# Kernel optimization log

Measured on AMD Instinct MI355X. Metric: run time of the kernel, lower is better.

The kernel has to match this reference:

```python
import jax, jax.numpy as jnp
import numpy as np

NUM_GRAPHS = 1024


def setup_inputs() -> dict:
    key = jax.random.key(0)
    k1, k2, k3, k4 = jax.random.split(key, 4)
    N, D = 1000000, 128
    node_embeddings = jax.random.normal(k1, (N, D), dtype=jnp.float32)
    batch_idx = jnp.sort(jax.random.randint(k2, (N,), 0, NUM_GRAPHS))
    # gate MLP params (Linear(D,D) -> ReLU -> Linear(D,1)), scaled like kaiming-ish init
    W1 = jax.random.normal(k3, (D, D), dtype=jnp.float32) / np.sqrt(D)
    b1 = jnp.zeros((D,), dtype=jnp.float32)
    W2 = jax.random.normal(k4, (D, 1), dtype=jnp.float32) / np.sqrt(D)
    b2 = jnp.zeros((1,), dtype=jnp.float32)
    return {"node_embeddings": node_embeddings, "batch_idx": batch_idx,
            "W1": W1, "b1": b1, "W2": W2, "b2": b2}


def reference(node_embeddings, batch_idx, W1, b1, W2, b2):
    # gate = sigmoid(Linear(ReLU(Linear(x))))  -> [N, 1]
    h = jax.nn.relu(node_embeddings @ W1 + b1)          # [N, D]
    gate = jax.nn.sigmoid(h @ W2 + b2)                   # [N, 1]
    gated = gate * node_embeddings                       # [N, D]
    # scatter-sum over batch_idx -> per-graph embedding [B, D]
    graph_embedding = jax.ops.segment_sum(gated, batch_idx, num_segments=NUM_GRAPHS)
    return graph_embedding
```

## Files before the change

### kernel.cpp

```cpp
#include <hip/hip_runtime.h>
#include <stdint.h>

#define D 128
#define TM 64
#define GRID 512
#define NTHREADS 512
#define PPW 9

typedef float f32x4 __attribute__((ext_vector_type(4)));
typedef short s16x8 __attribute__((ext_vector_type(8)));
typedef uint32_t u32x2 __attribute__((ext_vector_type(2)));

__device__ __forceinline__ short f2bf(float f) {
    union { float f; uint32_t u; } v; v.f = f;
    return (short)((v.u + 0x7fffu + ((v.u >> 16) & 1u)) >> 16);
}
__device__ __forceinline__ uint32_t cvt_pk_bf16(float lo, float hi) {
    uint32_t r;
    asm("v_cvt_pk_bf16_f32 %0, %1, %2" : "=v"(r) : "v"(lo), "v"(hi));
    return r;
}

__global__ __launch_bounds__(NTHREADS, 2)
void gate_agg_kernel(const float* __restrict__ X,
                     const int* __restrict__ bidx,
                     const float* __restrict__ W1,
                     const float* __restrict__ b1,
                     const float* __restrict__ W2,
                     const float* __restrict__ b2,
                     float* __restrict__ out,
                     int NT)
{
    __shared__ short xt[2][TM * D];
    __shared__ float pp[64 * PPW];
    __shared__ u32x2 gid[TM];

    const int tid = threadIdx.x;
    const int l = tid & 63;
    const int w = tid >> 6;
    const int l15 = l & 15;
    const int lk = l >> 4;

    s16x8 bfr[4];
    #pragma unroll
    for (int kt = 0; kt < 4; ++kt)
        #pragma unroll
        for (int e = 0; e < 8; ++e)
            bfr[kt][e] = f2bf(W1[(kt * 32 + lk * 8 + e) * D + 16 * w + l15]);

    float b1v[4], w2v[4];
    #pragma unroll
    for (int r = 0; r < 4; ++r) {
        b1v[r] = b1[16 * w + lk * 4 + r];
        w2v[r] = W2[16 * w + lk * 4 + r];
    }
    const float b2s = b2[0];

    const int q = NT / GRID, rem = NT % GRID;
    int t0, t1;
    if ((int)blockIdx.x < rem) { t0 = blockIdx.x * (q + 1); t1 = t0 + q + 1; }
    else { t0 = rem * (q + 1) + ((int)blockIdx.x - rem) * q; t1 = t0 + q; }

    float acc3[2] = {0.f, 0.f};
    int cur = -1;

    f32x4 vA[4], vB[4];
    int ridxA = 0, ridxB = 0;
    if (t0 < t1) {
        const float* xg = X + (size_t)t0 * TM * D;
        #pragma unroll
        for (int j = 0; j < 4; ++j) vA[j] = *(const f32x4*)(xg + (size_t)(j * 512 + tid) * 4);
        if (l < 8) ridxA = bidx[(size_t)t0 * TM + 8 * w + l];
    }
    if (t0 + 1 < t1) {
        const float* xg = X + (size_t)(t0 + 1) * TM * D;
        #pragma unroll
        for (int j = 0; j < 4; ++j) vB[j] = *(const f32x4*)(xg + (size_t)(j * 512 + tid) * 4);
        if (l < 8) ridxB = bidx[(size_t)(t0 + 1) * TM + 8 * w + l];
    }

#define BODY(V, RIDX, PB)                                                        \
    {                                                                            \
             \
        _Pragma("unroll")                                                        \
        for (int j = 0; j < 4; ++j) {                                            \
            int qc = j * 512 + tid;                                              \
            int row = qc >> 5, cq = qc & 31;                                     \
            int c2 = cq >> 1, h = cq & 1;                                        \
            u32x2 wv;                                                            \
            wv[0] = cvt_pk_bf16(V[j][0], V[j][1]);                               \
            wv[1] = cvt_pk_bf16(V[j][2], V[j][3]);                               \
            *(u32x2*)((char*)xt[PB] + row * 256 + ((c2 ^ (row & 15)) << 4) + h * 8) = wv; \
        }                                                                        \
        const int ridx_cur = RIDX;                                               \
          \
        if (t + 2 < t1) {                                                        \
            const float* xg = X + (size_t)(t + 2) * TM * D;                      \
            _Pragma("unroll")                                                    \
            for (int j = 0; j < 4; ++j)                                          \
                V[j] = *(const f32x4*)(xg + (size_t)(j * 512 + tid) * 4);        \
            if (l < 8) RIDX = bidx[(size_t)(t + 2) * TM + 8 * w + l];            \
        }                                                                        \
        asm volatile("s_waitcnt lgkmcnt(0)" ::: "memory");                       \
        __builtin_amdgcn_s_barrier();                               \
        __builtin_amdgcn_sched_barrier(0);                                       \
                \
        f32x4 acc[4];                                                            \
        acc[0] = (f32x4)0.f; acc[1] = (f32x4)0.f;                                \
        acc[2] = (f32x4)0.f; acc[3] = (f32x4)0.f;                                \
        _Pragma("unroll")                                                        \
        for (int kt = 0; kt < 4; ++kt) {                                         \
            const int kc = kt * 4 + lk;                                          \
            _Pragma("unroll")                                                    \
            for (int nf = 0; nf < 4; ++nf) {                                     \
                const int R = nf * 16 + l15;                                     \
                s16x8 xb = *(const s16x8*)((const char*)xt[PB] + R * 256 + ((kc ^ l15) << 4)); \
                acc[nf] = __builtin_amdgcn_mfma_f32_16x16x32_bf16(bfr[kt], xb, acc[nf], 0, 0, 0); \
            }                                                                    \
        }                                                                        \
          \
        _Pragma("unroll")                                                        \
        for (int nf = 0; nf < 4; ++nf) {                                         \
            float s = 0.f;                                                       \
            _Pragma("unroll")                                                    \
            for (int r = 0; r < 4; ++r) {                                        \
                float h = acc[nf][r] + b1v[r];                                   \
                h = fmaxf(h, 0.f);                                               \
                s = fmaf(h, w2v[r], s);                                          \
            }                                                                    \
            s += __shfl_xor(s, 16, 64);                                          \
            s += __shfl_xor(s, 32, 64);                                          \
            if (l < 16) pp[(nf * 16 + l) * PPW + w] = s;                         \
        }                                                                        \
        asm volatile("s_waitcnt lgkmcnt(0)" ::: "memory");                       \
        __builtin_amdgcn_s_barrier();                                  \
        __builtin_amdgcn_sched_barrier(0);                                       \
         \
        if (l < 8) {                                                             \
            const int node = 8 * w + l;                                          \
            float s = 0.f;                                                       \
            _Pragma("unroll")                                                    \
            for (int c = 0; c < 8; ++c) s += pp[node * PPW + c];                 \
            float g = 1.f / (1.f + __expf(-(s + b2s)));                          \
            u32x2 gi; gi[0] = __float_as_uint(g); gi[1] = (uint32_t)ridx_cur;    \
            gid[node] = gi;                                                      \
        }                                                                        \
        asm volatile("s_waitcnt lgkmcnt(0)" ::: "memory");    \
        __builtin_amdgcn_sched_barrier(0);                                       \
           \
        _Pragma("unroll")                                                        \
        for (int r = 0; r < 8; ++r) {                                            \
            const int row = 8 * w + r;                                           \
            u32x2 gi = gid[row];                                                 \
            const int seg = (int)gi[1];                                          \
            const float g = __uint_as_float(gi[0]);                              \
            if (seg != cur) {                                                    \
                if (cur >= 0) {                                                  \
                    atomicAdd(out + (size_t)cur * D + 2 * l,     acc3[0]);       \
                    atomicAdd(out + (size_t)cur * D + 2 * l + 1, acc3[1]);       \
                }                                                                \
                acc3[0] = 0.f; acc3[1] = 0.f; cur = seg;                         \
            }                                                                    \
            uint32_t xv = *(const uint32_t*)((const char*)xt[PB] + row * 256 +   \
                           ((((l >> 2) ^ (row & 15)) << 4)) + (l & 3) * 4);      \
            acc3[0] = fmaf(g, __uint_as_float(xv << 16),         acc3[0]);       \
            acc3[1] = fmaf(g, __uint_as_float(xv & 0xffff0000u), acc3[1]);       \
        }                                                                        \
    }

    int t = t0;
    while (t < t1) {
        BODY(vA, ridxA, 0);
        ++t; if (t >= t1) break;
        BODY(vB, ridxB, 1);
        ++t;
    }
#undef BODY

    if (cur >= 0) {
        atomicAdd(out + (size_t)cur * D + 2 * l,     acc3[0]);
        atomicAdd(out + (size_t)cur * D + 2 * l + 1, acc3[1]);
    }
}

extern "C" void kernel_launch(void* const* d_in, const int* in_sizes, int n_in,
                              void* d_out, int out_size, void* d_ws, size_t ws_size,
                              hipStream_t stream) {
    const float* X    = (const float*)d_in[0];
    const int*   bidx = (const int*)d_in[1];
    const float* W1   = (const float*)d_in[2];
    const float* b1   = (const float*)d_in[3];
    const float* W2   = (const float*)d_in[4];
    const float* b2   = (const float*)d_in[5];
    float* out = (float*)d_out;

    const int N  = in_sizes[0] / D;
    const int NT = N / TM;

    hipMemsetAsync(d_out, 0, (size_t)out_size * sizeof(float), stream);
    gate_agg_kernel<<<GRID, NTHREADS, 0, stream>>>(X, bidx, W1, b1, W2, b2, out, NT);
}
```

Before: 110.7 us.

## Retile gate GEMM so each wave covers 32 hidden units and 32 nodes

```diff
diff --git a/kernel.cpp b/kernel.cpp
--- a/kernel.cpp
+++ b/kernel.cpp
@@ -38,22 +38,28 @@
     const int tid = threadIdx.x;
     const int l = tid & 63;
     const int w = tid >> 6;
+    const int hb = w & 3;
+    const int nh = w >> 2;
     const int l15 = l & 15;
     const int lk = l >> 4;
 
-    s16x8 bfr[4];
+    s16x8 bfr[2][4];
     #pragma unroll
-    for (int kt = 0; kt < 4; ++kt)
-        #pragma unroll
-        for (int e = 0; e < 8; ++e)
-            bfr[kt][e] = f2bf(W1[(kt * 32 + lk * 8 + e) * D + 16 * w + l15]);
-
-    float b1v[4], w2v[4];
+    for (int j = 0; j < 2; ++j)
+        #pragma unroll
+        for (int kt = 0; kt < 4; ++kt)
+            #pragma unroll
+            for (int e = 0; e < 8; ++e)
+                bfr[j][kt][e] = f2bf(W1[(kt * 32 + lk * 8 + e) * D + 32 * hb + j * 16 + l15]);
+
+    float b1v[2][4], w2v[2][4];
     #pragma unroll
-    for (int r = 0; r < 4; ++r) {
-        b1v[r] = b1[16 * w + lk * 4 + r];
-        w2v[r] = W2[16 * w + lk * 4 + r];
-    }
+    for (int j = 0; j < 2; ++j)
+        #pragma unroll
+        for (int r = 0; r < 4; ++r) {
+            b1v[j][r] = b1[32 * hb + j * 16 + lk * 4 + r];
+            w2v[j][r] = W2[32 * hb + j * 16 + lk * 4 + r];
+        }
     const float b2s = b2[0];
 
     const int q = NT / GRID, rem = NT % GRID;
@@ -104,43 +110,46 @@
         asm volatile("s_waitcnt lgkmcnt(0)" ::: "memory");                       \
         __builtin_amdgcn_s_barrier();                               \
         __builtin_amdgcn_sched_barrier(0);                                       \
-                \
-        f32x4 acc[4];                                                            \
-        acc[0] = (f32x4)0.f; acc[1] = (f32x4)0.f;                                \
-        acc[2] = (f32x4)0.f; acc[3] = (f32x4)0.f;                                \
+         \
+        f32x4 acc[2][2];                                                         \
+        acc[0][0] = (f32x4)0.f; acc[0][1] = (f32x4)0.f;                          \
+        acc[1][0] = (f32x4)0.f; acc[1][1] = (f32x4)0.f;                          \
         _Pragma("unroll")                                                        \
         for (int kt = 0; kt < 4; ++kt) {                                         \
             const int kc = kt * 4 + lk;                                          \
             _Pragma("unroll")                                                    \
-            for (int nf = 0; nf < 4; ++nf) {                                     \
-                const int R = nf * 16 + l15;                                     \
+            for (int nf = 0; nf < 2; ++nf) {                                     \
+                const int R = 32 * nh + nf * 16 + l15;                           \
                 s16x8 xb = *(const s16x8*)((const char*)xt[PB] + R * 256 + ((kc ^ l15) << 4)); \
-                acc[nf] = __builtin_amdgcn_mfma_f32_16x16x32_bf16(bfr[kt], xb, acc[nf], 0, 0, 0); \
+                acc[nf][0] = __builtin_amdgcn_mfma_f32_16x16x32_bf16(bfr[0][kt], xb, acc[nf][0], 0, 0, 0); \
+                acc[nf][1] = __builtin_amdgcn_mfma_f32_16x16x32_bf16(bfr[1][kt], xb, acc[nf][1], 0, 0, 0); \
             }                                                                    \
         }                                                                        \
           \
         _Pragma("unroll")                                                        \
-        for (int nf = 0; nf < 4; ++nf) {                                         \
+        for (int nf = 0; nf < 2; ++nf) {                                         \
             float s = 0.f;                                                       \
             _Pragma("unroll")                                                    \
-            for (int r = 0; r < 4; ++r) {                                        \
-                float h = acc[nf][r] + b1v[r];                                   \
-                h = fmaxf(h, 0.f);                                               \
-                s = fmaf(h, w2v[r], s);                                          \
-            }                                                                    \
+            for (int j = 0; j < 2; ++j)                                          \
+                _Pragma("unroll")                                                \
+                for (int r = 0; r < 4; ++r) {                                    \
+                    float h = acc[nf][j][r] + b1v[j][r];                         \
+                    h = fmaxf(h, 0.f);                                           \
+                    s = fmaf(h, w2v[j][r], s);                                   \
+                }                                                                \
             s += __shfl_xor(s, 16, 64);                                          \
             s += __shfl_xor(s, 32, 64);                                          \
-            if (l < 16) pp[(nf * 16 + l) * PPW + w] = s;                         \
+            if (l < 16) pp[(32 * nh + nf * 16 + l) * PPW + hb] = s;              \
         }                                                                        \
         asm volatile("s_waitcnt lgkmcnt(0)" ::: "memory");                       \
         __builtin_amdgcn_s_barrier();                                  \
         __builtin_amdgcn_sched_barrier(0);                                       \
-         \
+        \
         if (l < 8) {                                                             \
             const int node = 8 * w + l;                                          \
             float s = 0.f;                                                       \
             _Pragma("unroll")                                                    \
-            for (int c = 0; c < 8; ++c) s += pp[node * PPW + c];                 \
+            for (int c = 0; c < 4; ++c) s += pp[node * PPW + c];                 \
             float g = 1.f / (1.f + __expf(-(s + b2s)));                          \
             u32x2 gi; gi[0] = __float_as_uint(g); gi[1] = (uint32_t)ridx_cur;    \
             gid[node] = gi;                                                      \
```

Measured after the change: 113.9 us. 1.03x slower.

## Process two tiles per iteration with quad-buffered LDS to halve barriers

Applied to the files above, without the earlier changes.

```diff
diff --git a/kernel.cpp b/kernel.cpp
--- a/kernel.cpp
+++ b/kernel.cpp
@@ -31,9 +31,9 @@
                      float* __restrict__ out,
                      int NT)
 {
-    __shared__ short xt[2][TM * D];
-    __shared__ float pp[64 * PPW];
-    __shared__ u32x2 gid[TM];
+    __shared__ short xt[4][TM * D];
+    __shared__ float pp[2][64 * PPW];
+    __shared__ u32x2 gid[2][TM];
 
     const int tid = threadIdx.x;
     const int l = tid & 63;
@@ -79,9 +79,7 @@
         if (l < 8) ridxB = bidx[(size_t)(t0 + 1) * TM + 8 * w + l];
     }
 
-#define BODY(V, RIDX, PB)                                                        \
-    {                                                                            \
-             \
+#define STAGE(V, SB) {                                                           \
         _Pragma("unroll")                                                        \
         for (int j = 0; j < 4; ++j) {                                            \
             int qc = j * 512 + tid;                                              \
@@ -90,21 +88,20 @@
             u32x2 wv;                                                            \
             wv[0] = cvt_pk_bf16(V[j][0], V[j][1]);                               \
             wv[1] = cvt_pk_bf16(V[j][2], V[j][3]);                               \
-            *(u32x2*)((char*)xt[PB] + row * 256 + ((c2 ^ (row & 15)) << 4) + h * 8) = wv; \
-        }                                                                        \
-        const int ridx_cur = RIDX;                                               \
-          \
-        if (t + 2 < t1) {                                                        \
-            const float* xg = X + (size_t)(t + 2) * TM * D;                      \
-            _Pragma("unroll")                                                    \
-            for (int j = 0; j < 4; ++j)                                          \
-                V[j] = *(const f32x4*)(xg + (size_t)(j * 512 + tid) * 4);        \
-            if (l < 8) RIDX = bidx[(size_t)(t + 2) * TM + 8 * w + l];            \
-        }                                                                        \
-        asm volatile("s_waitcnt lgkmcnt(0)" ::: "memory");                       \
-        __builtin_amdgcn_s_barrier();                               \
-        __builtin_amdgcn_sched_barrier(0);                                       \
-                \
+            *(u32x2*)((char*)xt + (SB) * 16384 + row * 256 +                     \
+                      ((c2 ^ (row & 15)) << 4) + h * 8) = wv;                    \
+        }                                                                        \
+    }
+
+#define ISSUE(V, RIDX, TT) {                                                     \
+        const float* xg = X + (size_t)(TT) * TM * D;                             \
+        _Pragma("unroll")                                                        \
+        for (int j = 0; j < 4; ++j)                                              \
+            V[j] = *(const f32x4*)(xg + (size_t)(j * 512 + tid) * 4);            \
+        if (l < 8) RIDX = bidx[(size_t)(TT) * TM + 8 * w + l];                   \
+    }
+
+#define MFMA_PP(SB, PI) {                                                        \
         f32x4 acc[4];                                                            \
         acc[0] = (f32x4)0.f; acc[1] = (f32x4)0.f;                                \
         acc[2] = (f32x4)0.f; acc[3] = (f32x4)0.f;                                \
@@ -114,11 +111,11 @@
             _Pragma("unroll")                                                    \
             for (int nf = 0; nf < 4; ++nf) {                                     \
                 const int R = nf * 16 + l15;                                     \
-                s16x8 xb = *(const s16x8*)((const char*)xt[PB] + R * 256 + ((kc ^ l15) << 4)); \
+                s16x8 xb = *(const s16x8*)((const char*)xt + (SB) * 16384 +      \
+                            R * 256 + ((kc ^ l15) << 4));                        \
                 acc[nf] = __builtin_amdgcn_mfma_f32_16x16x32_bf16(bfr[kt], xb, acc[nf], 0, 0, 0); \
             }                                                                    \
         }                                                                        \
-          \
         _Pragma("unroll")                                                        \
         for (int nf = 0; nf < 4; ++nf) {                                         \
             float s = 0.f;                                                       \
@@ -130,28 +127,27 @@
             }                                                                    \
             s += __shfl_xor(s, 16, 64);                                          \
             s += __shfl_xor(s, 32, 64);                                          \
-            if (l < 16) pp[(nf * 16 + l) * PPW + w] = s;                         \
-        }                                                                        \
-        asm volatile("s_waitcnt lgkmcnt(0)" ::: "memory");                       \
-        __builtin_amdgcn_s_barrier();                                  \
-        __builtin_amdgcn_sched_barrier(0);                                       \
-         \
+            if (l < 16) pp[PI][(nf * 16 + l) * PPW + w] = s;                     \
+        }                                                                        \
+    }
+
+#define GATE(PI, RCUR) {                                                         \
         if (l < 8) {                                                             \
             const int node = 8 * w + l;                                          \
             float s = 0.f;                                                       \
             _Pragma("unroll")                                                    \
-            for (int c = 0; c < 8; ++c) s += pp[node * PPW + c];                 \
+            for (int c = 0; c < 8; ++c) s += pp[PI][node * PPW + c];             \
             float g = 1.f / (1.f + __expf(-(s + b2s)));                          \
-            u32x2 gi; gi[0] = __float_as_uint(g); gi[1] = (uint32_t)ridx_cur;    \
-            gid[node] = gi;                                                      \
-        }                                                                        \
-        asm volatile("s_waitcnt lgkmcnt(0)" ::: "memory");    \
-        __builtin_amdgcn_sched_barrier(0);                                       \
-           \
+            u32x2 gi; gi[0] = __float_as_uint(g); gi[1] = (uint32_t)(RCUR);      \
+            gid[PI][node] = gi;                                                  \
+        }                                                                        \
+    }
+
+#define PHASE3(SB, PI) {                                                         \
         _Pragma("unroll")                                                        \
         for (int r = 0; r < 8; ++r) {                                            \
             const int row = 8 * w + r;                                           \
-            u32x2 gi = gid[row];                                                 \
+            u32x2 gi = gid[PI][row];                                             \
             const int seg = (int)gi[1];                                          \
             const float g = __uint_as_float(gi[0]);                              \
             if (seg != cur) {                                                    \
@@ -161,21 +157,60 @@
                 }                                                                \
                 acc3[0] = 0.f; acc3[1] = 0.f; cur = seg;                         \
             }                                                                    \
-            uint32_t xv = *(const uint32_t*)((const char*)xt[PB] + row * 256 +   \
-                           ((((l >> 2) ^ (row & 15)) << 4)) + (l & 3) * 4);      \
+            uint32_t xv = *(const uint32_t*)((const char*)xt + (SB) * 16384 +    \
+                           row * 256 + ((((l >> 2) ^ (row & 15)) << 4)) + (l & 3) * 4); \
             acc3[0] = fmaf(g, __uint_as_float(xv << 16),         acc3[0]);       \
             acc3[1] = fmaf(g, __uint_as_float(xv & 0xffff0000u), acc3[1]);       \
         }                                                                        \
     }
 
-    int t = t0;
-    while (t < t1) {
-        BODY(vA, ridxA, 0);
-        ++t; if (t >= t1) break;
-        BODY(vB, ridxB, 1);
-        ++t;
-    }
-#undef BODY
+    int t = t0, cb = 0;
+    while (t + 1 < t1) {
+        STAGE(vA, cb);
+        STAGE(vB, cb + 1);
+        const int rA = ridxA, rB = ridxB;
+        if (t + 2 < t1) ISSUE(vA, ridxA, t + 2);
+        if (t + 3 < t1) ISSUE(vB, ridxB, t + 3);
+        asm volatile("s_waitcnt lgkmcnt(0)" ::: "memory");
+        __builtin_amdgcn_s_barrier();
+        __builtin_amdgcn_sched_barrier(0);
+
+        MFMA_PP(cb, 0);
+        MFMA_PP(cb + 1, 1);
+        asm volatile("s_waitcnt lgkmcnt(0)" ::: "memory");
+        __builtin_amdgcn_s_barrier();
+        __builtin_amdgcn_sched_barrier(0);
+
+        GATE(0, rA);
+        GATE(1, rB);
+        asm volatile("s_waitcnt lgkmcnt(0)" ::: "memory");
+        __builtin_amdgcn_sched_barrier(0);
+
+        PHASE3(cb, 0);
+        PHASE3(cb + 1, 1);
+
+        t += 2; cb ^= 2;
+    }
+    if (t < t1) {
+        STAGE(vA, cb);
+        const int rA = ridxA;
+        asm volatile("s_waitcnt lgkmcnt(0)" ::: "memory");
+        __builtin_amdgcn_s_barrier();
+        __builtin_amdgcn_sched_barrier(0);
+        MFMA_PP(cb, 0);
+        asm volatile("s_waitcnt lgkmcnt(0)" ::: "memory");
+        __builtin_amdgcn_s_barrier();
+        __builtin_amdgcn_sched_barrier(0);
+        GATE(0, rA);
+        asm volatile("s_waitcnt lgkmcnt(0)" ::: "memory");
+        __builtin_amdgcn_sched_barrier(0);
+        PHASE3(cb, 0);
+    }
+#undef STAGE
+#undef ISSUE
+#undef MFMA_PP
+#undef GATE
+#undef PHASE3
 
     if (cur >= 0) {
         atomicAdd(out + (size_t)cur * D + 2 * l,     acc3[0]);
```

Measured after the change: 129.7 us. 1.17x slower.

## Software-pipeline gate and aggregation one tile behind MFMA with triple-buffered LDS

Applied to the files above, without the earlier changes.

```diff
diff --git a/kernel.cpp b/kernel.cpp
--- a/kernel.cpp
+++ b/kernel.cpp
@@ -31,8 +31,8 @@
                      float* __restrict__ out,
                      int NT)
 {
-    __shared__ short xt[2][TM * D];
-    __shared__ float pp[64 * PPW];
+    __shared__ short xt[3][TM * D];
+    __shared__ float pp[2][64 * PPW];
     __shared__ u32x2 gid[TM];
 
     const int tid = threadIdx.x;
@@ -79,9 +79,7 @@
         if (l < 8) ridxB = bidx[(size_t)(t0 + 1) * TM + 8 * w + l];
     }
 
-#define BODY(V, RIDX, PB)                                                        \
-    {                                                                            \
-             \
+#define STAGE(V, CB) {                                                           \
         _Pragma("unroll")                                                        \
         for (int j = 0; j < 4; ++j) {                                            \
             int qc = j * 512 + tid;                                              \
@@ -90,21 +88,12 @@
             u32x2 wv;                                                            \
             wv[0] = cvt_pk_bf16(V[j][0], V[j][1]);                               \
             wv[1] = cvt_pk_bf16(V[j][2], V[j][3]);                               \
-            *(u32x2*)((char*)xt[PB] + row * 256 + ((c2 ^ (row & 15)) << 4) + h * 8) = wv; \
-        }                                                                        \
-        const int ridx_cur = RIDX;                                               \
-          \
-        if (t + 2 < t1) {                                                        \
-            const float* xg = X + (size_t)(t + 2) * TM * D;                      \
-            _Pragma("unroll")                                                    \
-            for (int j = 0; j < 4; ++j)                                          \
-                V[j] = *(const f32x4*)(xg + (size_t)(j * 512 + tid) * 4);        \
-            if (l < 8) RIDX = bidx[(size_t)(t + 2) * TM + 8 * w + l];            \
-        }                                                                        \
-        asm volatile("s_waitcnt lgkmcnt(0)" ::: "memory");                       \
-        __builtin_amdgcn_s_barrier();                               \
-        __builtin_amdgcn_sched_barrier(0);                                       \
-                \
+            *(u32x2*)((char*)xt + (CB) * 16384 + row * 256 +                     \
+                      ((c2 ^ (row & 15)) << 4) + h * 8) = wv;                    \
+        }                                                                        \
+    }
+
+#define MFMA_PP(CB, PI) {                                                        \
         f32x4 acc[4];                                                            \
         acc[0] = (f32x4)0.f; acc[1] = (f32x4)0.f;                                \
         acc[2] = (f32x4)0.f; acc[3] = (f32x4)0.f;                                \
@@ -114,11 +103,11 @@
             _Pragma("unroll")                                                    \
             for (int nf = 0; nf < 4; ++nf) {                                     \
                 const int R = nf * 16 + l15;                                     \
-                s16x8 xb = *(const s16x8*)((const char*)xt[PB] + R * 256 + ((kc ^ l15) << 4)); \
+                s16x8 xb = *(const s16x8*)((const char*)xt + (CB) * 16384 +      \
+                            R * 256 + ((kc ^ l15) << 4));                        \
                 acc[nf] = __builtin_amdgcn_mfma_f32_16x16x32_bf16(bfr[kt], xb, acc[nf], 0, 0, 0); \
             }                                                                    \
         }                                                                        \
-          \
         _Pragma("unroll")                                                        \
         for (int nf = 0; nf < 4; ++nf) {                                         \
             float s = 0.f;                                                       \
@@ -130,24 +119,23 @@
             }                                                                    \
             s += __shfl_xor(s, 16, 64);                                          \
             s += __shfl_xor(s, 32, 64);                                          \
-            if (l < 16) pp[(nf * 16 + l) * PPW + w] = s;                         \
-        }                                                                        \
-        asm volatile("s_waitcnt lgkmcnt(0)" ::: "memory");                       \
-        __builtin_amdgcn_s_barrier();                                  \
-        __builtin_amdgcn_sched_barrier(0);                                       \
-         \
+            if (l < 16) pp[PI][(nf * 16 + l) * PPW + w] = s;                     \
+        }                                                                        \
+    }
+
+#define GATE(PI, RIDXP) {                                                        \
         if (l < 8) {                                                             \
             const int node = 8 * w + l;                                          \
             float s = 0.f;                                                       \
             _Pragma("unroll")                                                    \
-            for (int c = 0; c < 8; ++c) s += pp[node * PPW + c];                 \
+            for (int c = 0; c < 8; ++c) s += pp[PI][node * PPW + c];             \
             float g = 1.f / (1.f + __expf(-(s + b2s)));                          \
-            u32x2 gi; gi[0] = __float_as_uint(g); gi[1] = (uint32_t)ridx_cur;    \
+            u32x2 gi; gi[0] = __float_as_uint(g); gi[1] = (uint32_t)(RIDXP);     \
             gid[node] = gi;                                                      \
         }                                                                        \
-        asm volatile("s_waitcnt lgkmcnt(0)" ::: "memory");    \
-        __builtin_amdgcn_sched_barrier(0);                                       \
-           \
+    }
+
+#define PHASE3(CB) {                                                             \
         _Pragma("unroll")                                                        \
         for (int r = 0; r < 8; ++r) {                                            \
             const int row = 8 * w + r;                                           \
@@ -161,20 +149,54 @@
                 }                                                                \
                 acc3[0] = 0.f; acc3[1] = 0.f; cur = seg;                         \
             }                                                                    \
-            uint32_t xv = *(const uint32_t*)((const char*)xt[PB] + row * 256 +   \
-                           ((((l >> 2) ^ (row & 15)) << 4)) + (l & 3) * 4);      \
+            uint32_t xv = *(const uint32_t*)((const char*)xt + (CB) * 16384 +    \
+                           row * 256 + ((((l >> 2) ^ (row & 15)) << 4)) + (l & 3) * 4); \
             acc3[0] = fmaf(g, __uint_as_float(xv << 16),         acc3[0]);       \
             acc3[1] = fmaf(g, __uint_as_float(xv & 0xffff0000u), acc3[1]);       \
         }                                                                        \
     }
 
-    int t = t0;
+#define BODY(V, RIDX) {                                                          \
+        STAGE(V, cb);                                                            \
+        const int ridx_cur = RIDX;                                               \
+        if (t + 2 < t1) {                                    \
+            const float* xg = X + (size_t)(t + 2) * TM * D;                      \
+            _Pragma("unroll")                                                    \
+            for (int j = 0; j < 4; ++j)                                          \
+                V[j] = *(const f32x4*)(xg + (size_t)(j * 512 + tid) * 4);        \
+            if (l < 8) RIDX = bidx[(size_t)(t + 2) * TM + 8 * w + l];            \
+        }                                                                        \
+        asm volatile("s_waitcnt lgkmcnt(0)" ::: "memory");                       \
+        __builtin_amdgcn_s_barrier();                      \
+        __builtin_amdgcn_sched_barrier(0);                                       \
+        MFMA_PP(cb, t & 1);                                                      \
+        if (t > t0) {                                                            \
+            GATE((t - 1) & 1, ridxPrev);                                         \
+            asm volatile("s_waitcnt lgkmcnt(0)" ::: "memory");                   \
+            PHASE3(cbPrev);                                                      \
+        }                                                                        \
+        ridxPrev = ridx_cur;                                                     \
+        cbPrev = cb;                                                             \
+        cb = (cb == 2) ? 0 : cb + 1;                                             \
+    }
+
+    int t = t0, cb = 0, cbPrev = 0, ridxPrev = 0;
     while (t < t1) {
-        BODY(vA, ridxA, 0);
-        ++t; if (t >= t1) break;
-        BODY(vB, ridxB, 1);
-        ++t;
-    }
+        BODY(vA, ridxA); ++t; if (t >= t1) break;
+        BODY(vB, ridxB); ++t;
+    }
+    if (t1 > t0) {
+        asm volatile("s_waitcnt lgkmcnt(0)" ::: "memory");
+        __builtin_amdgcn_s_barrier();
+        __builtin_amdgcn_sched_barrier(0);
+        GATE((t1 - 1) & 1, ridxPrev);
+        asm volatile("s_waitcnt lgkmcnt(0)" ::: "memory");
+        PHASE3(cbPrev);
+    }
+#undef STAGE
+#undef MFMA_PP
+#undef GATE
+#undef PHASE3
 #undef BODY
 
     if (cur >= 0) {
```

Result: slower. 118.4 us (+7.0%).
